# Optimization experiments

Measured on AMD Instinct MI355X. Metric: run time of the kernel, lower is better.

The kernel has to match this reference:

```python
import jax, jax.numpy as jnp
import numpy as np

B, S, H, E, K = 4, 4096, 4096, 16, 2


def setup_inputs() -> dict:
    key = jax.random.key(0)
    k1, k2 = jax.random.split(key)
    x = jax.random.normal(k1, (B, S, H), dtype=jnp.float32)
    # nn.Linear(H, E, bias=False) weight has shape [E, H]
    W = jax.random.normal(k2, (E, H), dtype=jnp.float32) * (1.0 / np.sqrt(H))
    return {"x": x, "W": W}


def reference(x, W):
    num_experts = W.shape[0]
    top_k = K
    # gate GEMM: [B,S,H] @ [H,E] -> [B,S,E]
    router_logits = jnp.einsum("bsh,eh->bse", x, W)
    router_probs = jax.nn.softmax(router_logits, axis=-1)
    top_k_probs, expert_indices = jax.lax.top_k(router_probs, top_k)  # [B,S,K]
    top_k_probs = top_k_probs / jnp.sum(top_k_probs, axis=-1, keepdims=True)
    # one_hot [B,S,K,E] -> sum over K -> [B,S,E] -> mean over batch -> [S,E]
    tokens_per_expert = jax.nn.one_hot(expert_indices, num_experts, dtype=jnp.float32).sum(-2).mean(0)
    avg_prob_per_expert = router_probs.mean(axis=(0, 1))  # [E]
    aux_loss = num_experts * jnp.sum(tokens_per_expert * avg_prob_per_expert)
    return (top_k_probs, expert_indices, aux_loss)
```

## Files before the change

### kernel.cpp

```cpp
#include <hip/hip_runtime.h>
#include <math.h>

namespace {
constexpr int kB = 4;
constexpr int kS = 4096;
constexpr int kH = 4096;
constexpr int kE = 16;
constexpr int kTokens = kB * kS;
constexpr int kT = 4;
constexpr int kEW = 8;
constexpr int kThreads = 256;
constexpr int kTokBlk = 8;
constexpr int kGrid = kTokens / kTokBlk;
constexpr int kChunk = 256;
constexpr int kNC = kH / kChunk;
}

__global__ __launch_bounds__(kThreads) void router_main(
    const float* __restrict__ x, const float* __restrict__ W,
    float* __restrict__ out_probs,
    float* __restrict__ out_idx,
    float* __restrict__ gpart) {
  __shared__ float s_logit[kTokBlk][kE];
  __shared__ float s_cnt[kE];
  __shared__ float s_psum[kE];

  const int tid = threadIdx.x;
  const int wave = tid >> 6;
  const int lane = tid & 63;
  const int tg = wave >> 1;
  const int eo = (wave & 1) * kEW;
  const int tokBase = blockIdx.x * kTokBlk;
  const int tok0 = tokBase + tg * kT;

  if (tid < kE) { s_cnt[tid] = 0.f; s_psum[tid] = 0.f; }

  const float* xb = x + (size_t)tok0 * kH + lane * 4;
  const float* wb = W + (size_t)eo * kH + lane * 4;

  float acc[kT][kEW];
#pragma unroll
  for (int t = 0; t < kT; ++t)
#pragma unroll
    for (int e = 0; e < kEW; ++e) acc[t][e] = 0.f;

  for (int j = 0; j < kNC; ++j) {
    const size_t off = (size_t)j * kChunk;
    float4 xv[kT];
#pragma unroll
    for (int t = 0; t < kT; ++t)
      xv[t] = *reinterpret_cast<const float4*>(xb + (size_t)t * kH + off);
    float4 wv[kEW];
#pragma unroll
    for (int e = 0; e < kEW; ++e)
      wv[e] = *reinterpret_cast<const float4*>(wb + (size_t)e * kH + off);
#pragma unroll
    for (int e = 0; e < kEW; ++e)
#pragma unroll
      for (int t = 0; t < kT; ++t) {
        acc[t][e] = fmaf(xv[t].x, wv[e].x, acc[t][e]);
        acc[t][e] = fmaf(xv[t].y, wv[e].y, acc[t][e]);
        acc[t][e] = fmaf(xv[t].z, wv[e].z, acc[t][e]);
        acc[t][e] = fmaf(xv[t].w, wv[e].w, acc[t][e]);
      }
  }

#pragma unroll
  for (int off = 1; off < 64; off <<= 1) {
#pragma unroll
    for (int t = 0; t < kT; ++t)
#pragma unroll
      for (int e = 0; e < kEW; ++e)
        acc[t][e] += __shfl_xor(acc[t][e], off, 64);
  }

  if (lane < kT) {
    const int r = tg * kT + lane;
#pragma unroll
    for (int e = 0; e < kEW; ++e) s_logit[r][eo + e] = acc[lane][e];
  }
  __syncthreads();

  if (wave == 0 && lane < kTokBlk) {
    const int tok = tokBase + lane;
    float l[kE];
#pragma unroll
    for (int e = 0; e < kE; ++e) l[e] = s_logit[lane][e];

    float m = l[0];
#pragma unroll
    for (int e = 1; e < kE; ++e) m = fmaxf(m, l[e]);
    float p[kE];
    float s = 0.f;
#pragma unroll
    for (int e = 0; e < kE; ++e) { p[e] = __expf(l[e] - m); s += p[e]; }
    const float inv = 1.f / s;
#pragma unroll
    for (int e = 0; e < kE; ++e) p[e] *= inv;

    int i1 = 0;
    float v1 = p[0];
#pragma unroll
    for (int e = 1; e < kE; ++e)
      if (p[e] > v1) { v1 = p[e]; i1 = e; }
    int i2 = (i1 == 0) ? 1 : 0;
    float v2 = p[i2];
#pragma unroll
    for (int e = 0; e < kE; ++e) {
      if (e == i1) continue;
      if (p[e] > v2) { v2 = p[e]; i2 = e; }
    }

    const float ns = 1.f / (v1 + v2);
    out_probs[tok * 2 + 0] = v1 * ns;
    out_probs[tok * 2 + 1] = v2 * ns;
    out_idx[tok * 2 + 0] = (float)i1;
    out_idx[tok * 2 + 1] = (float)i2;

#pragma unroll
    for (int e = 0; e < kE; ++e) atomicAdd(&s_psum[e], p[e]);
    atomicAdd(&s_cnt[i1], 1.f);
    atomicAdd(&s_cnt[i2], 1.f);
  }
  __syncthreads();
  if (tid < 2 * kE)
    gpart[(size_t)blockIdx.x * 2 * kE + tid] =
        (tid < kE) ? s_cnt[tid] : s_psum[tid - kE];
}

__global__ __launch_bounds__(1024) void aux_finish(
    const float* __restrict__ gpart, float* __restrict__ out_aux) {
  __shared__ float s_red[32][32];
  __shared__ float s_final[32];
  const int tid = threadIdx.x;
  const int c = tid & 31;
  const int r0 = tid >> 5;
  float s = 0.f;
  for (int k = 0; k < kGrid / 32; ++k)
    s += gpart[(size_t)(r0 * (kGrid / 32) + k) * 32 + c];
  s_red[r0][c] = s;
  __syncthreads();
  if (tid < 32) {
    float t = 0.f;
    for (int r = 0; r < 32; ++r) t += s_red[r][tid];
    s_final[tid] = t;
  }
  __syncthreads();
  if (tid == 0) {
    double acc = 0.0;
    for (int e = 0; e < kE; ++e)
      acc += (double)s_final[e] * (double)s_final[kE + e];
    out_aux[0] = (float)(acc * (double)kE / ((double)kB * (double)kB * (double)kS));
  }
}

extern "C" void kernel_launch(void* const* d_in, const int* in_sizes, int n_in,
                              void* d_out, int out_size, void* d_ws, size_t ws_size,
                              hipStream_t stream) {
  const float* x = (const float*)d_in[0];
  const float* W = (const float*)d_in[1];
  float* out = (float*)d_out;
  float* gpart = (float*)d_ws;

  router_main<<<kGrid, kThreads, 0, stream>>>(
      x, W, out, out + 2 * kTokens, gpart);
  aux_finish<<<1, 1024, 0, stream>>>(gpart, out + 4 * kTokens);
}
```

Before: 88.11 us.

## Software-pipeline x and W loads with triple-buffered registers and manual waitcnt

Result: slower. 104.5 us (+18.6%).

```diff
diff --git a/kernel.cpp b/kernel.cpp
--- a/kernel.cpp
+++ b/kernel.cpp
@@ -44,26 +44,74 @@
 #pragma unroll
     for (int e = 0; e < kEW; ++e) acc[t][e] = 0.f;
 
-  for (int j = 0; j < kNC; ++j) {
+  float4 xv0[kT], xv1[kT], xv2[kT];
+  float4 wvA[4], wvB[4];
+
+  auto issue_x = [&](int j, float4 (&xv)[kT]) {
     const size_t off = (size_t)j * kChunk;
-    float4 xv[kT];
 #pragma unroll
     for (int t = 0; t < kT; ++t)
       xv[t] = *reinterpret_cast<const float4*>(xb + (size_t)t * kH + off);
-    float4 wv[kEW];
-#pragma unroll
-    for (int e = 0; e < kEW; ++e)
-      wv[e] = *reinterpret_cast<const float4*>(wb + (size_t)e * kH + off);
-#pragma unroll
-    for (int e = 0; e < kEW; ++e)
+  };
+  auto issue_wA = [&](int j) {
+    const size_t off = (size_t)j * kChunk;
+#pragma unroll
+    for (int e = 0; e < 4; ++e)
+      wvA[e] = *reinterpret_cast<const float4*>(wb + (size_t)e * kH + off);
+  };
+  auto issue_wB = [&](int j) {
+    const size_t off = (size_t)j * kChunk;
+#pragma unroll
+    for (int e = 0; e < 4; ++e)
+      wvB[e] = *reinterpret_cast<const float4*>(wb + (size_t)(4 + e) * kH + off);
+  };
+
+  issue_wA(0);
+  issue_wB(0);
+  asm volatile("" ::: "memory");
+  issue_x(0, xv0);
+  asm volatile("" ::: "memory");
+  issue_x(1, xv1);
+  asm volatile("s_waitcnt vmcnt(4)" ::: "memory");
+
+  auto body = [&](int j, const float4 (&cur)[kT], float4 (&nxt2)[kT]) {
+#pragma unroll
+    for (int e = 0; e < 4; ++e)
 #pragma unroll
       for (int t = 0; t < kT; ++t) {
-        acc[t][e] = fmaf(xv[t].x, wv[e].x, acc[t][e]);
-        acc[t][e] = fmaf(xv[t].y, wv[e].y, acc[t][e]);
-        acc[t][e] = fmaf(xv[t].z, wv[e].z, acc[t][e]);
-        acc[t][e] = fmaf(xv[t].w, wv[e].w, acc[t][e]);
+        acc[t][e] = fmaf(cur[t].x, wvA[e].x, acc[t][e]);
+        acc[t][e] = fmaf(cur[t].y, wvA[e].y, acc[t][e]);
+        acc[t][e] = fmaf(cur[t].z, wvA[e].z, acc[t][e]);
+        acc[t][e] = fmaf(cur[t].w, wvA[e].w, acc[t][e]);
       }
-  }
+    if (j + 1 < kNC) issue_wA(j + 1);
+    asm volatile("" ::: "memory");
+#pragma unroll
+    for (int e = 0; e < 4; ++e)
+#pragma unroll
+      for (int t = 0; t < kT; ++t) {
+        acc[t][4 + e] = fmaf(cur[t].x, wvB[e].x, acc[t][4 + e]);
+        acc[t][4 + e] = fmaf(cur[t].y, wvB[e].y, acc[t][4 + e]);
+        acc[t][4 + e] = fmaf(cur[t].z, wvB[e].z, acc[t][4 + e]);
+        acc[t][4 + e] = fmaf(cur[t].w, wvB[e].w, acc[t][4 + e]);
+      }
+    if (j + 1 < kNC) issue_wB(j + 1);
+    asm volatile("" ::: "memory");
+    if (j + 2 < kNC) {
+      issue_x(j + 2, nxt2);
+      asm volatile("s_waitcnt vmcnt(4)" ::: "memory");
+    } else if (j + 1 < kNC) {
+      asm volatile("s_waitcnt vmcnt(0)" ::: "memory");
+    }
+  };
+
+#pragma unroll 1
+  for (int jj = 0; jj < kNC - 1; jj += 3) {
+    body(jj + 0, xv0, xv2);
+    body(jj + 1, xv1, xv0);
+    body(jj + 2, xv2, xv1);
+  }
+  body(kNC - 1, xv0, xv2);
 
 #pragma unroll
   for (int off = 1; off < 64; off <<= 1) {
```

## Compute all 16 experts per wave and drop shared-memory logit exchange

Applied to the files above, without the earlier changes.

Result: slower. 115.6 us (+31.2%).

```diff
diff --git a/kernel.cpp b/kernel.cpp
--- a/kernel.cpp
+++ b/kernel.cpp
@@ -8,41 +8,38 @@
 constexpr int kE = 16;
 constexpr int kTokens = kB * kS;
 constexpr int kT = 4;
-constexpr int kEW = 8;
-constexpr int kThreads = 256;
-constexpr int kTokBlk = 8;
+constexpr int kWaves = 4;
+constexpr int kThreads = 64 * kWaves;
+constexpr int kTokBlk = kT * kWaves;
 constexpr int kGrid = kTokens / kTokBlk;
 constexpr int kChunk = 256;
 constexpr int kNC = kH / kChunk;
 }
 
-__global__ __launch_bounds__(kThreads) void router_main(
+__global__ __attribute__((amdgpu_waves_per_eu(4, 4)))
+__launch_bounds__(kThreads) void router_main(
     const float* __restrict__ x, const float* __restrict__ W,
     float* __restrict__ out_probs,
     float* __restrict__ out_idx,
     float* __restrict__ gpart) {
-  __shared__ float s_logit[kTokBlk][kE];
   __shared__ float s_cnt[kE];
   __shared__ float s_psum[kE];
 
   const int tid = threadIdx.x;
   const int wave = tid >> 6;
   const int lane = tid & 63;
-  const int tg = wave >> 1;
-  const int eo = (wave & 1) * kEW;
-  const int tokBase = blockIdx.x * kTokBlk;
-  const int tok0 = tokBase + tg * kT;
+  const int tok0 = blockIdx.x * kTokBlk + wave * kT;
 
   if (tid < kE) { s_cnt[tid] = 0.f; s_psum[tid] = 0.f; }
 
   const float* xb = x + (size_t)tok0 * kH + lane * 4;
-  const float* wb = W + (size_t)eo * kH + lane * 4;
+  const float* wb = W + lane * 4;
 
-  float acc[kT][kEW];
+  float acc[kT][kE];
 #pragma unroll
   for (int t = 0; t < kT; ++t)
 #pragma unroll
-    for (int e = 0; e < kEW; ++e) acc[t][e] = 0.f;
+    for (int e = 0; e < kE; ++e) acc[t][e] = 0.f;
 
   for (int j = 0; j < kNC; ++j) {
     const size_t off = (size_t)j * kChunk;
@@ -50,19 +47,25 @@
 #pragma unroll
     for (int t = 0; t < kT; ++t)
       xv[t] = *reinterpret_cast<const float4*>(xb + (size_t)t * kH + off);
-    float4 wv[kEW];
 #pragma unroll
-    for (int e = 0; e < kEW; ++e)
-      wv[e] = *reinterpret_cast<const float4*>(wb + (size_t)e * kH + off);
+    for (int p = 0; p < 4; ++p) {
+      float4 wv[4];
 #pragma unroll
-    for (int e = 0; e < kEW; ++e)
+      for (int e = 0; e < 4; ++e)
+        wv[e] = *reinterpret_cast<const float4*>(
+            wb + (size_t)(p * 4 + e) * kH + off);
 #pragma unroll
-      for (int t = 0; t < kT; ++t) {
-        acc[t][e] = fmaf(xv[t].x, wv[e].x, acc[t][e]);
-        acc[t][e] = fmaf(xv[t].y, wv[e].y, acc[t][e]);
-        acc[t][e] = fmaf(xv[t].z, wv[e].z, acc[t][e]);
-        acc[t][e] = fmaf(xv[t].w, wv[e].w, acc[t][e]);
+      for (int e = 0; e < 4; ++e) {
+        const int ei = p * 4 + e;
+#pragma unroll
+        for (int t = 0; t < kT; ++t) {
+          acc[t][ei] = fmaf(xv[t].x, wv[e].x, acc[t][ei]);
+          acc[t][ei] = fmaf(xv[t].y, wv[e].y, acc[t][ei]);
+          acc[t][ei] = fmaf(xv[t].z, wv[e].z, acc[t][ei]);
+          acc[t][ei] = fmaf(xv[t].w, wv[e].w, acc[t][ei]);
+        }
       }
+    }
   }
 
 #pragma unroll
@@ -70,22 +73,17 @@
 #pragma unroll
     for (int t = 0; t < kT; ++t)
 #pragma unroll
-      for (int e = 0; e < kEW; ++e)
+      for (int e = 0; e < kE; ++e)
         acc[t][e] += __shfl_xor(acc[t][e], off, 64);
   }
 
-  if (lane < kT) {
-    const int r = tg * kT + lane;
-#pragma unroll
-    for (int e = 0; e < kEW; ++e) s_logit[r][eo + e] = acc[lane][e];
-  }
   __syncthreads();
 
-  if (wave == 0 && lane < kTokBlk) {
-    const int tok = tokBase + lane;
+  if (lane < kT) {
+    const int tok = tok0 + lane;
     float l[kE];
 #pragma unroll
-    for (int e = 0; e < kE; ++e) l[e] = s_logit[lane][e];
+    for (int e = 0; e < kE; ++e) l[e] = acc[lane][e];
 
     float m = l[0];
 #pragma unroll
```
